# Kernel optimization log

Measured on AMD Instinct MI355X. Metric: run time of the kernel, lower is better.

The kernel has to match this reference:

```python
import jax, jax.numpy as jnp
import numpy as np

H = 128          # hid_feats
IN0, IN1 = 128, 64
OUT = 64         # out_feats
L = 3            # num_layers
N = 50000        # nodes per graph


def _rbf(x, W, b):
    # sklearn RBFSampler: z = sqrt(2/D) * cos(x @ W + b)
    return jnp.sqrt(2.0 / H) * jnp.cos(x @ W + b)


def _sage_branch(feat, src, dst, Wself, Wneigh, bias, n_nodes):
    # deg of each dst node (constant across layers)
    deg = jax.ops.segment_sum(jnp.ones_like(dst, dtype=feat.dtype), dst, n_nodes)
    denom = jnp.maximum(deg, 1.0)[:, None]
    for i in range(Wself.shape[0]):
        s = jax.ops.segment_sum(feat[src], dst, n_nodes)   # gather + scatter-add
        neigh = jnp.where(deg[:, None] > 0, s / denom, 0.0)
        feat = feat @ Wself[i] + neigh @ Wneigh[i] + bias[i]
    return feat


def setup_inputs() -> dict:
    key = jax.random.key(0)
    ks = jax.random.split(key, 20)
    gamma = 0.1
    inp = {}
    inp['feat0'] = jax.random.normal(ks[0], (N, IN0), jnp.float32)
    inp['feat1'] = jax.random.normal(ks[1], (N, IN1), jnp.float32)
    E = 800000
    inp['src0'] = jax.random.randint(ks[2], (E,), 0, N, jnp.int32)
    inp['dst0'] = jax.random.randint(ks[3], (E,), 0, N, jnp.int32)
    inp['src1'] = jax.random.randint(ks[4], (E,), 0, N, jnp.int32)
    inp['dst1'] = jax.random.randint(ks[5], (E,), 0, N, jnp.int32)
    # RBF random Fourier feature params (W ~ sqrt(2*gamma)*N(0,1), b ~ U[0,2pi))
    inp['rbf_W0'] = jnp.sqrt(2 * gamma) * jax.random.normal(ks[6], (IN0, H), jnp.float32)
    inp['rbf_b0'] = jax.random.uniform(ks[7], (H,), jnp.float32, 0.0, 2 * np.pi)
    inp['rbf_W1'] = jnp.sqrt(2 * gamma) * jax.random.normal(ks[8], (IN1, H), jnp.float32)
    inp['rbf_b1'] = jax.random.uniform(ks[9], (H,), jnp.float32, 0.0, 2 * np.pi)
    sc = 1.0 / np.sqrt(H)
    # branch 1 (g1) and branch 2 (g0) SAGEConv params, stacked over layers
    inp['Wself1'] = sc * jax.random.normal(ks[10], (L, H, H), jnp.float32)
    inp['Wneigh1'] = sc * jax.random.normal(ks[11], (L, H, H), jnp.float32)
    inp['b1'] = jnp.zeros((L, H), jnp.float32)
    inp['Wself2'] = sc * jax.random.normal(ks[12], (L, H, H), jnp.float32)
    inp['Wneigh2'] = sc * jax.random.normal(ks[13], (L, H, H), jnp.float32)
    inp['b2'] = jnp.zeros((L, H), jnp.float32)
    inp['fc1_W'] = sc * jax.random.normal(ks[14], (2 * H, H), jnp.float32)
    inp['fc1_b'] = jnp.zeros((H,), jnp.float32)
    inp['out_W'] = sc * jax.random.normal(ks[15], (H, OUT), jnp.float32)
    inp['out_b'] = jnp.zeros((OUT,), jnp.float32)
    inp['ro_W'] = (1.0 / np.sqrt(OUT)) * jax.random.normal(ks[16], (OUT, 1), jnp.float32)
    inp['ro_b'] = jnp.zeros((1,), jnp.float32)
    return inp


def reference(feat0, feat1, src0, dst0, src1, dst1,
              rbf_W0, rbf_b0, rbf_W1, rbf_b1,
              Wself1, Wneigh1, b1, Wself2, Wneigh2, b2,
              fc1_W, fc1_b, out_W, out_b, ro_W, ro_b):
    # branch 1: g1 path-complex features
    h1 = _rbf(feat1, rbf_W1, rbf_b1)
    y1 = _sage_branch(h1, src1, dst1, Wself1, Wneigh1, b1, feat1.shape[0])
    # branch 2: g0 node features
    h0 = _rbf(feat0, rbf_W0, rbf_b0)
    y2 = _sage_branch(h0, src0, dst0, Wself2, Wneigh2, b2, feat0.shape[0])
    # adaptive_avg_pool1d to 1 == mean over nodes
    y = jnp.concatenate([y2.mean(axis=0), y1.mean(axis=0)], axis=0)  # [2H]
    h = jax.nn.relu(y @ fc1_W + fc1_b)          # dropout is identity in eval
    h = jax.nn.leaky_relu(h @ out_W + out_b, negative_slope=0.01)
    return h @ ro_W + ro_b                      # [1]
```

## Files before the change

### kernel.cpp

```cpp
#include <hip/hip_runtime.h>
#include <math.h>

#define HF   128
#define CAPW 64
#define HB   64

__global__ __launch_bounds__(256) void hist_kernel(const int* __restrict__ s0, const int* __restrict__ d0,
                                                   const int* __restrict__ s1, const int* __restrict__ d1,
                                                   unsigned int* __restrict__ cntbuf,
                                                   int N, int E){
  __shared__ unsigned int sm32[12544];
  const int t = threadIdx.x;
  const int HW = (N + 3) >> 2;
  const int b  = blockIdx.x & 63;
  const int br = (blockIdx.x >> 6) & 1;
  const int z  = blockIdx.x >> 7;
  const int* keys = z ? (br ? d1 : d0) : (br ? s1 : s0);
  for (int w = t; w < HW; w += 256) sm32[w] = 0u;
  __syncthreads();
  const int C  = (E + HB - 1) / HB;
  const int lo = b * C;
  int hi = lo + C; if (hi > E) hi = E;
  for (int i = lo + t; i < hi; i += 256){
    int k = keys[i];
    atomicAdd(&sm32[k >> 2], 1u << ((k & 3) << 3));
  }
  __syncthreads();
  unsigned int* out = cntbuf + ((size_t)(z * 2 + br) * HB + b) * HW;
  for (int w = t; w < HW; w += 256) out[w] = sm32[w];
}

__global__ __launch_bounds__(256) void scan_kernel(unsigned int* __restrict__ cntbuf,
                                                   int* __restrict__ deg,
                                                   int* __restrict__ fill, int N){
  int k = blockIdx.x * 256 + threadIdx.x;
  if (k >= 2 * N) return;
  const int br = k >= N;
  const int kk = k - br * N;
  const int HW = (N + 3) >> 2;
  unsigned char* cb = (unsigned char*)cntbuf;
  size_t dbase = ((size_t)(2 + br) * HB) * HW * 4 + kk;
  int ds = 0;
  for (int b = 0; b < HB; ++b) ds += cb[dbase + (size_t)b * HW * 4];
  deg[k] = ds;
  size_t sbase = ((size_t)(0 + br) * HB) * HW * 4 + kk;
  int run = 0;
  for (int b = 0; b < HB; ++b){
    size_t a = sbase + (size_t)b * HW * 4;
    int c = cb[a];
    cb[a] = (unsigned char)run;
    run += c;
  }
  fill[k] = run;
}

__global__ __launch_bounds__(256) void scatter_kernel(const int* __restrict__ s0, const int* __restrict__ d0,
                                                      const int* __restrict__ s1, const int* __restrict__ d1,
                                                      const unsigned int* __restrict__ cntbuf,
                                                      unsigned short* __restrict__ slots,
                                                      int N, int E){
  __shared__ unsigned int sm32[12544];
  const int t  = threadIdx.x;
  const int b  = blockIdx.x & 63;
  const int br = blockIdx.x >> 6;
  const int HW = (N + 3) >> 2;
  const unsigned int* offw = cntbuf + ((size_t)br * HB + b) * HW;
  for (int w = t; w < HW; w += 256) sm32[w] = offw[w];
  __syncthreads();
  const int* srcA = br ? s1 : s0;
  const int* dstA = br ? d1 : d0;
  const int C  = (E + HB - 1) / HB;
  const int lo = b * C;
  int hi = lo + C; if (hi > E) hi = E;
  const size_t obase = (size_t)br * N;
  for (int i = lo + t; i < hi; i += 256){
    int s = srcA[i];
    int d = dstA[i];
    unsigned int old = atomicAdd(&sm32[s >> 2], 1u << ((s & 3) << 3));
    int j = (old >> ((s & 3) << 3)) & 0xff;
    if (j < CAPW) slots[(obase + s) * CAPW + j] = (unsigned short)d;
  }
}

__global__ __launch_bounds__(256) void pull1_kernel(const unsigned short* __restrict__ slots,
                                                    const int* __restrict__ fill,
                                                    const int* __restrict__ deg,
                                                    float* __restrict__ w1,
                                                    float* __restrict__ qa,
                                                    double* __restrict__ S, int N){
  int i = blockIdx.x * 256 + threadIdx.x;
  int t = threadIdx.x;
  float a = 0.f;
  int dgi = 0;
  int br = 0;
  bool valid = i < 2 * N;
  if (valid){
    br = i >= N;
    int o = br * N;
    int c = fill[i]; if (c > CAPW) c = CAPW;
    const unsigned short* sl = slots + (size_t)i * CAPW;
    int j = 0;
    for (; j + 7 < c; j += 8){
      int dA = sl[j], dB = sl[j+1], dC = sl[j+2], dD = sl[j+3];
      int dE = sl[j+4], dF = sl[j+5], dG = sl[j+6], dH = sl[j+7];
      a += 1.f/(float)deg[o+dA] + 1.f/(float)deg[o+dB]
         + 1.f/(float)deg[o+dC] + 1.f/(float)deg[o+dD]
         + 1.f/(float)deg[o+dE] + 1.f/(float)deg[o+dF]
         + 1.f/(float)deg[o+dG] + 1.f/(float)deg[o+dH];
    }
    for (; j < c; ++j) a += 1.f/(float)deg[o + sl[j]];
    dgi = deg[i];
    w1[i] = a;
    qa[i] = dgi > 0 ? a * (1.f/(float)dgi) : 0.f;
  }
  __shared__ double rd[4][256];
  bool pos = valid && dgi > 0;
  rd[0][t] = (pos && !br) ? 1.0 : 0.0;
  rd[1][t] = (pos && !br) ? (double)a : 0.0;
  rd[2][t] = (pos &&  br) ? 1.0 : 0.0;
  rd[3][t] = (pos &&  br) ? (double)a : 0.0;
  __syncthreads();
  for (int off = 128; off; off >>= 1){
    if (t < off){
      rd[0][t] += rd[0][t+off]; rd[1][t] += rd[1][t+off];
      rd[2][t] += rd[2][t+off]; rd[3][t] += rd[3][t+off];
    }
    __syncthreads();
  }
  if (t < 4) atomicAdd(&S[t], rd[t][0]);
}

template<bool WQ>
__global__ __launch_bounds__(256) void pull_kernel(const unsigned short* __restrict__ slots,
                                                   const int* __restrict__ fill,
                                                   const int* __restrict__ deg,
                                                   const float* __restrict__ qin,
                                                   float* __restrict__ wout,
                                                   float* __restrict__ qout, int N){
  int i = blockIdx.x * 256 + threadIdx.x;
  if (i >= 2 * N) return;
  int br = i >= N;
  int o = br * N;
  int c = fill[i]; if (c > CAPW) c = CAPW;
  const unsigned short* sl = slots + (size_t)i * CAPW;
  float a = 0.f;
  int j = 0;
  for (; j + 7 < c; j += 8){
    int dA = sl[j], dB = sl[j+1], dC = sl[j+2], dD = sl[j+3];
    int dE = sl[j+4], dF = sl[j+5], dG = sl[j+6], dH = sl[j+7];
    a += qin[o+dA] + qin[o+dB] + qin[o+dC] + qin[o+dD]
       + qin[o+dE] + qin[o+dF] + qin[o+dG] + qin[o+dH];
  }
  for (; j < c; ++j) a += qin[o + sl[j]];
  wout[i] = a;
  if (WQ){
    int dgi = deg[i];
    qout[i] = dgi > 0 ? a * (1.f/(float)dgi) : 0.f;
  }
}

template<int K1>
__device__ __forceinline__ void gemmred_body(const float* __restrict__ A,
                                             const float* __restrict__ W,
                                             const float* __restrict__ bias,
                                             const float* __restrict__ w1,
                                             const float* __restrict__ w2,
                                             const float* __restrict__ w3,
                                             int wo, float* __restrict__ partial,
                                             int rb, int N,
                                             float (*As)[68], float (*Bs)[132], float (*red)[128]){
  const int t  = threadIdx.x;
  const int tx = t & 15;
  const int ty = t >> 4;
  const int rowbase = rb << 6;

  float acc[4][8];
  #pragma unroll
  for (int i = 0; i < 4; ++i)
    #pragma unroll
    for (int j = 0; j < 8; ++j) acc[i][j] = 0.f;

  const int ar = t >> 2;
  const int ac = (t & 3) << 2;
  const int arow = rowbase + ar;
  const int bk0 = t >> 5;
  const int bc0 = (t & 31) << 2;

  for (int k0 = 0; k0 < K1; k0 += 16){
    __syncthreads();
    float4 av = make_float4(0.f, 0.f, 0.f, 0.f);
    if (arow < N) av = *(const float4*)&A[(size_t)arow * K1 + (k0 + ac)];
    As[ac + 0][ar] = av.x; As[ac + 1][ar] = av.y;
    As[ac + 2][ar] = av.z; As[ac + 3][ar] = av.w;
    float4 b0 = *(const float4*)&W[(size_t)(k0 + bk0) * HF + bc0];
    float4 b1 = *(const float4*)&W[(size_t)(k0 + bk0 + 8) * HF + bc0];
    *(float4*)&Bs[bk0][bc0]     = b0;
    *(float4*)&Bs[bk0 + 8][bc0] = b1;
    __syncthreads();
    #pragma unroll
    for (int kk = 0; kk < 16; ++kk){
      const float4 a  = *(const float4*)&As[kk][ty << 2];
      const float4 p0 = *(const float4*)&Bs[kk][tx << 2];
      const float4 p1 = *(const float4*)&Bs[kk][64 + (tx << 2)];
      const float aa[4] = {a.x, a.y, a.z, a.w};
      const float bb[8] = {p0.x, p0.y, p0.z, p0.w, p1.x, p1.y, p1.z, p1.w};
      #pragma unroll
      for (int i = 0; i < 4; ++i)
        #pragma unroll
        for (int j = 0; j < 8; ++j)
          acc[i][j] = fmaf(aa[i], bb[j], acc[i][j]);
    }
  }

  const float4 bia0 = *(const float4*)&bias[tx << 2];
  const float4 bia1 = *(const float4*)&bias[64 + (tx << 2)];
  const float bb0[8] = {bia0.x, bia0.y, bia0.z, bia0.w, bia1.x, bia1.y, bia1.z, bia1.w};
  float o[4][8];
  float wr[4][4];
  #pragma unroll
  for (int i = 0; i < 4; ++i){
    int row = rowbase + (ty << 2) + i;
    bool valid = row < N;
    #pragma unroll
    for (int j = 0; j < 8; ++j)
      o[i][j] = 0.125f * cosf(acc[i][j] + bb0[j]);
    wr[0][i] = valid ? 1.f : 0.f;
    wr[1][i] = valid ? w1[wo + row] : 0.f;
    wr[2][i] = valid ? w2[wo + row] : 0.f;
    wr[3][i] = valid ? w3[wo + row] : 0.f;
  }
  __syncthreads();
  #pragma unroll
  for (int k = 0; k < 4; ++k){
    float cw[8];
    #pragma unroll
    for (int j = 0; j < 8; ++j)
      cw[j] = wr[k][0]*o[0][j] + wr[k][1]*o[1][j] + wr[k][2]*o[2][j] + wr[k][3]*o[3][j];
    #pragma unroll
    for (int j = 0; j < 4; ++j){
      red[ty][(tx << 2) + j]      = cw[j];
      red[ty][64 + (tx << 2) + j] = cw[4 + j];
    }
    __syncthreads();
    for (int off = 8; off; off >>= 1){
      if (ty < off){
        #pragma unroll
        for (int j = 0; j < 4; ++j){
          red[ty][(tx << 2) + j]      += red[ty + off][(tx << 2) + j];
          red[ty][64 + (tx << 2) + j] += red[ty + off][64 + (tx << 2) + j];
        }
      }
      __syncthreads();
    }
    if (ty == 0){
      #pragma unroll
      for (int j = 0; j < 4; ++j){
        partial[(size_t)rb * 512 + k * 128 + (tx << 2) + j]      = red[0][(tx << 2) + j];
        partial[(size_t)rb * 512 + k * 128 + 64 + (tx << 2) + j] = red[0][64 + (tx << 2) + j];
      }
    }
    __syncthreads();
  }
}

__global__ __launch_bounds__(256) void gemmred2_kernel(const float* __restrict__ A0,
                                                       const float* __restrict__ W0,
                                                       const float* __restrict__ b0,
                                                       const float* __restrict__ A1,
                                                       const float* __restrict__ W1,
                                                       const float* __restrict__ b1,
                                                       const float* __restrict__ w1,
                                                       const float* __restrict__ w2,
                                                       const float* __restrict__ w3,
                                                       float* __restrict__ partial,
                                                       int N, int gg){
  __shared__ __align__(16) float smem[3200];
  float (*As)[68]   = (float(*)[68])smem;
  float (*Bs)[132]  = (float(*)[132])(smem + 1088);
  float (*red)[128] = (float(*)[128])smem;
  if ((int)blockIdx.x < gg)
    gemmred_body<128>(A0, W0, b0, w1, w2, w3, 0, partial, blockIdx.x, N, As, Bs, red);
  else
    gemmred_body<64>(A1, W1, b1, w1, w2, w3, N, partial + (size_t)gg * 512,
                     blockIdx.x - gg, N, As, Bs, red);
}

__global__ __launch_bounds__(512) void greduce_kernel(const float* __restrict__ partial,
                                                      double* __restrict__ G, int nb, int stride){
  int br = blockIdx.y;
  const float* p = partial + (size_t)br * stride;
  double* Gb = G + 512 * br;
  int t = threadIdx.x;
  double s = 0.0;
  for (int b = blockIdx.x; b < nb; b += gridDim.x) s += (double)p[(size_t)b * 512 + t];
  atomicAdd(&Gb[t], s);
}

__global__ __launch_bounds__(512) void head_kernel(const double* __restrict__ G,
                                                   const double* __restrict__ S,
                                                   const float* __restrict__ WsA, const float* __restrict__ WnA, const float* __restrict__ bA,
                                                   const float* __restrict__ WsB, const float* __restrict__ WnB, const float* __restrict__ bB,
                                                   float* __restrict__ ymean, int n){
  const int br = blockIdx.x;
  const double* Gb = G + 512 * br;
  const double* Sb = S + 2 * br;
  const float* Ws   = br ? WsB : WsA;
  const float* Wn   = br ? WnB : WnA;
  const float* bias = br ? bB  : bA;
  float* yout = ymean + 128 * br;

  __shared__ double g[4][128], ng[3][128];
  __shared__ float lws[32][128], lwn[32][128];
  const int t = threadIdx.x;
  const int k = t >> 7, j = t & 127;
  g[k][j] = Gb[t];
  double s[4];
  s[0] = (double)n; s[1] = Sb[0]; s[2] = Sb[1]; s[3] = 0.0;

  for (int i = 0; i < 3; ++i){
    const float* ws = Ws + (size_t)i * 16384;
    const float* wn = Wn + (size_t)i * 16384;
    const float* bi = bias + (size_t)i * 128;
    const int kmax = 2 - i;
    double a = (k <= kmax) ? s[k] * (double)bi[j] : 0.0;
    for (int mc = 0; mc < 128; mc += 32){
      __syncthreads();
      #pragma unroll
      for (int pp = 0; pp < 2; ++pp){
        int idx = (pp * 512 + t) << 2;
        int mm = idx >> 7, cc = idx & 127;
        *(float4*)&lws[mm][cc] = *(const float4*)&ws[(size_t)(mc + mm) * 128 + cc];
        *(float4*)&lwn[mm][cc] = *(const float4*)&wn[(size_t)(mc + mm) * 128 + cc];
      }
      __syncthreads();
      if (k <= kmax){
        #pragma unroll
        for (int m = 0; m < 32; ++m){
          a += g[k][mc + m]     * (double)lws[m][j];
          a += g[k + 1][mc + m] * (double)lwn[m][j];
        }
      }
    }
    __syncthreads();
    if (k <= kmax) ng[k][j] = a;
    __syncthreads();
    if (k <= kmax) g[k][j] = ng[k][j];
  }
  __syncthreads();
  if (t < 128) yout[t] = (float)(g[0][t] / (double)n);
}

__global__ void final_kernel(const float* __restrict__ ymean,
                             const float* __restrict__ fc1W, const float* __restrict__ fc1b,
                             const float* __restrict__ outW, const float* __restrict__ outb,
                             const float* __restrict__ roW, const float* __restrict__ rob,
                             float* __restrict__ out){
  __shared__ float y[256], h1[128], h2[64];
  int t = threadIdx.x;
  y[t] = ymean[t];
  __syncthreads();
  if (t < 128){
    float a = fc1b[t];
    for (int k = 0; k < 256; ++k) a = fmaf(y[k], fc1W[k * 128 + t], a);
    h1[t] = a > 0.f ? a : 0.f;
  }
  __syncthreads();
  if (t < 64){
    float a = outb[t];
    for (int k = 0; k < 128; ++k) a = fmaf(h1[k], outW[k * 64 + t], a);
    h2[t] = a > 0.f ? a : 0.01f * a;
  }
  __syncthreads();
  if (t == 0){
    float a = rob[0];
    for (int k = 0; k < 64; ++k) a = fmaf(h2[k], roW[k], a);
    out[0] = a;
  }
}

extern "C" void kernel_launch(void* const* d_in, const int* in_sizes, int n_in,
                              void* d_out, int out_size, void* d_ws, size_t ws_size,
                              hipStream_t stream){
  const float* feat0  = (const float*)d_in[0];
  const float* feat1  = (const float*)d_in[1];
  const int*   src0   = (const int*)d_in[2];
  const int*   dst0   = (const int*)d_in[3];
  const int*   src1   = (const int*)d_in[4];
  const int*   dst1   = (const int*)d_in[5];
  const float* rbfW0  = (const float*)d_in[6];
  const float* rbfb0  = (const float*)d_in[7];
  const float* rbfW1  = (const float*)d_in[8];
  const float* rbfb1  = (const float*)d_in[9];
  const float* Wself1 = (const float*)d_in[10];
  const float* Wneigh1= (const float*)d_in[11];
  const float* b1     = (const float*)d_in[12];
  const float* Wself2 = (const float*)d_in[13];
  const float* Wneigh2= (const float*)d_in[14];
  const float* b2     = (const float*)d_in[15];
  const float* fc1W   = (const float*)d_in[16];
  const float* fc1b   = (const float*)d_in[17];
  const float* outW   = (const float*)d_in[18];
  const float* outb   = (const float*)d_in[19];
  const float* roW    = (const float*)d_in[20];
  const float* rob    = (const float*)d_in[21];

  const int N = in_sizes[0] / 128;
  const int E = in_sizes[2];
  const int HW = (N + 3) >> 2;

  char* w = (char*)d_ws;
  size_t off = 0;
  auto alloc = [&](size_t bytes) -> char* {
    char* p = w + off; off += (bytes + 255) & ~(size_t)255; return p;
  };
  int*    deg    = (int*)   alloc((size_t)2 * N * 4);
  int*    fill   = (int*)   alloc((size_t)2 * N * 4);
  float*  w1     = (float*) alloc((size_t)2 * N * 4);
  float*  w2     = (float*) alloc((size_t)2 * N * 4);
  float*  w3     = (float*) alloc((size_t)2 * N * 4);
  float*  qa     = (float*) alloc((size_t)2 * N * 4);
  float*  qb     = (float*) alloc((size_t)2 * N * 4);
  double* S      = (double*)alloc(4 * sizeof(double));
  double* G      = (double*)alloc(1024 * sizeof(double));
  float*  ymean  = (float*) alloc(256 * sizeof(float));
  const int gg   = (N + 63) >> 6;
  float*  partial= (float*) alloc((size_t)2 * gg * 512 * 4);
  unsigned short* slots = (unsigned short*)alloc((size_t)2 * N * CAPW * 2);
  unsigned int* cntbuf  = (unsigned int*)alloc((size_t)4 * HB * HW * 4);

  const size_t slen = (size_t)((char*)ymean - (char*)S);

  const int nGrid2 = (2 * N + 255) >> 8;

  hipMemsetAsync(S, 0, slen, stream);
  hist_kernel<<<256, 256, 0, stream>>>(src0, dst0, src1, dst1, cntbuf, N, E);
  scan_kernel<<<nGrid2, 256, 0, stream>>>(cntbuf, deg, fill, N);
  scatter_kernel<<<128, 256, 0, stream>>>(src0, dst0, src1, dst1, cntbuf, slots, N, E);
  pull1_kernel<<<nGrid2, 256, 0, stream>>>(slots, fill, deg, w1, qa, S, N);
  pull_kernel<true ><<<nGrid2, 256, 0, stream>>>(slots, fill, deg, qa, w2, qb, N);
  pull_kernel<false><<<nGrid2, 256, 0, stream>>>(slots, fill, deg, qb, w3, qb, N);
  gemmred2_kernel<<<2 * gg, 256, 0, stream>>>(feat0, rbfW0, rbfb0, feat1, rbfW1, rbfb1,
                                              w1, w2, w3, partial, N, gg);
  greduce_kernel<<<dim3(16, 2), 512, 0, stream>>>(partial, G, gg, gg * 512);
  head_kernel<<<2, 512, 0, stream>>>(G, S, Wself2, Wneigh2, b2, Wself1, Wneigh1, b1, ymean, N);
  final_kernel<<<1, 256, 0, stream>>>(ymean, fc1W, fc1b, outW, outb, roW, rob, (float*)d_out);
}
```

Before: 216.2 us.

## Split scatter by source-key halves and enlarge RBF GEMM tile to 128 rows

The scatter kernel now launches twice as many blocks, and each block handles only half of the source-node key range. This halves the shared-memory offset table, which should allow more resident blocks, at the cost of every block reading all edges and skipping those outside its half. The fused RBF GEMM+reduction now processes 128-row tiles with an 8x8 per-thread accumulator, and the weighted reduction is accumulated directly in registers. This halves the number of partial blocks and gives more FMA work per shared-memory load, but raises register pressure.

```diff
diff --git a/kernel.cpp b/kernel.cpp
--- a/kernel.cpp
+++ b/kernel.cpp
@@ -59,13 +59,18 @@
                                                       const unsigned int* __restrict__ cntbuf,
                                                       unsigned short* __restrict__ slots,
                                                       int N, int E){
-  __shared__ unsigned int sm32[12544];
+  __shared__ unsigned int sm32[6272];
   const int t  = threadIdx.x;
   const int b  = blockIdx.x & 63;
-  const int br = blockIdx.x >> 6;
+  const int br = (blockIdx.x >> 6) & 1;
+  const int h  = blockIdx.x >> 7;
   const int HW = (N + 3) >> 2;
-  const unsigned int* offw = cntbuf + ((size_t)br * HB + b) * HW;
-  for (int w = t; w < HW; w += 256) sm32[w] = offw[w];
+  const int HN = ((N + 7) >> 3) << 2;
+  const int klo = h ? HN : 0;
+  const int khi = h ? N : HN;
+  const int nw  = (khi - klo + 3) >> 2;
+  const unsigned int* offw = cntbuf + ((size_t)br * HB + b) * HW + (klo >> 2);
+  for (int w = t; w < nw; w += 256) sm32[w] = offw[w];
   __syncthreads();
   const int* srcA = br ? s1 : s0;
   const int* dstA = br ? d1 : d0;
@@ -75,9 +80,11 @@
   const size_t obase = (size_t)br * N;
   for (int i = lo + t; i < hi; i += 256){
     int s = srcA[i];
+    if (s < klo || s >= khi) continue;
     int d = dstA[i];
-    unsigned int old = atomicAdd(&sm32[s >> 2], 1u << ((s & 3) << 3));
-    int j = (old >> ((s & 3) << 3)) & 0xff;
+    int sl = s - klo;
+    unsigned int old = atomicAdd(&sm32[sl >> 2], 1u << ((sl & 3) << 3));
+    int j = (old >> ((sl & 3) << 3)) & 0xff;
     if (j < CAPW) slots[(obase + s) * CAPW + j] = (unsigned short)d;
   }
 }
@@ -168,44 +175,50 @@
                                              const float* __restrict__ w3,
                                              int wo, float* __restrict__ partial,
                                              int rb, int N,
-                                             float (*As)[68], float (*Bs)[132], float (*red)[128]){
+                                             float (*As)[132], float (*Bs)[132], float (*red)[128]){
   const int t  = threadIdx.x;
   const int tx = t & 15;
   const int ty = t >> 4;
-  const int rowbase = rb << 6;
-
-  float acc[4][8];
+  const int rowbase = rb << 7;
+
+  float acc[8][8];
   #pragma unroll
-  for (int i = 0; i < 4; ++i)
+  for (int i = 0; i < 8; ++i)
     #pragma unroll
     for (int j = 0; j < 8; ++j) acc[i][j] = 0.f;
 
-  const int ar = t >> 2;
-  const int ac = (t & 3) << 2;
+  const int ar  = t >> 1;
+  const int ac8 = (t & 1) << 3;
   const int arow = rowbase + ar;
-  const int bk0 = t >> 5;
-  const int bc0 = (t & 31) << 2;
+  const int bk0 = t >> 4;
+  const int bc0 = (t & 15) << 3;
 
   for (int k0 = 0; k0 < K1; k0 += 16){
     __syncthreads();
-    float4 av = make_float4(0.f, 0.f, 0.f, 0.f);
-    if (arow < N) av = *(const float4*)&A[(size_t)arow * K1 + (k0 + ac)];
-    As[ac + 0][ar] = av.x; As[ac + 1][ar] = av.y;
-    As[ac + 2][ar] = av.z; As[ac + 3][ar] = av.w;
+    float4 av0 = make_float4(0.f,0.f,0.f,0.f), av1 = make_float4(0.f,0.f,0.f,0.f);
+    if (arow < N){
+      av0 = *(const float4*)&A[(size_t)arow * K1 + (k0 + ac8)];
+      av1 = *(const float4*)&A[(size_t)arow * K1 + (k0 + ac8 + 4)];
+    }
+    As[ac8 + 0][ar] = av0.x; As[ac8 + 1][ar] = av0.y;
+    As[ac8 + 2][ar] = av0.z; As[ac8 + 3][ar] = av0.w;
+    As[ac8 + 4][ar] = av1.x; As[ac8 + 5][ar] = av1.y;
+    As[ac8 + 6][ar] = av1.z; As[ac8 + 7][ar] = av1.w;
     float4 b0 = *(const float4*)&W[(size_t)(k0 + bk0) * HF + bc0];
-    float4 b1 = *(const float4*)&W[(size_t)(k0 + bk0 + 8) * HF + bc0];
+    float4 b1 = *(const float4*)&W[(size_t)(k0 + bk0) * HF + bc0 + 4];
     *(float4*)&Bs[bk0][bc0]     = b0;
-    *(float4*)&Bs[bk0 + 8][bc0] = b1;
+    *(float4*)&Bs[bk0][bc0 + 4] = b1;
     __syncthreads();
     #pragma unroll
     for (int kk = 0; kk < 16; ++kk){
-      const float4 a  = *(const float4*)&As[kk][ty << 2];
+      const float4 a0 = *(const float4*)&As[kk][ty << 2];
+      const float4 a1 = *(const float4*)&As[kk][64 + (ty << 2)];
       const float4 p0 = *(const float4*)&Bs[kk][tx << 2];
       const float4 p1 = *(const float4*)&Bs[kk][64 + (tx << 2)];
-      const float aa[4] = {a.x, a.y, a.z, a.w};
+      const float aa[8] = {a0.x, a0.y, a0.z, a0.w, a1.x, a1.y, a1.z, a1.w};
       const float bb[8] = {p0.x, p0.y, p0.z, p0.w, p1.x, p1.y, p1.z, p1.w};
       #pragma unroll
-      for (int i = 0; i < 4; ++i)
+      for (int i = 0; i < 8; ++i)
         #pragma unroll
         for (int j = 0; j < 8; ++j)
           acc[i][j] = fmaf(aa[i], bb[j], acc[i][j]);
@@ -215,31 +228,35 @@
   const float4 bia0 = *(const float4*)&bias[tx << 2];
   const float4 bia1 = *(const float4*)&bias[64 + (tx << 2)];
   const float bb0[8] = {bia0.x, bia0.y, bia0.z, bia0.w, bia1.x, bia1.y, bia1.z, bia1.w};
-  float o[4][8];
-  float wr[4][4];
+  float cw[4][8];
   #pragma unroll
-  for (int i = 0; i < 4; ++i){
-    int row = rowbase + (ty << 2) + i;
+  for (int k = 0; k < 4; ++k)
+    #pragma unroll
+    for (int j = 0; j < 8; ++j) cw[k][j] = 0.f;
+  #pragma unroll
+  for (int i = 0; i < 8; ++i){
+    int row = rowbase + (i < 4 ? (ty << 2) + i : 64 + (ty << 2) + (i - 4));
     bool valid = row < N;
+    float wk0 = valid ? 1.f : 0.f;
+    float wk1 = valid ? w1[wo + row] : 0.f;
+    float wk2 = valid ? w2[wo + row] : 0.f;
+    float wk3 = valid ? w3[wo + row] : 0.f;
     #pragma unroll
-    for (int j = 0; j < 8; ++j)
-      o[i][j] = 0.125f * cosf(acc[i][j] + bb0[j]);
-    wr[0][i] = valid ? 1.f : 0.f;
-    wr[1][i] = valid ? w1[wo + row] : 0.f;
-    wr[2][i] = valid ? w2[wo + row] : 0.f;
-    wr[3][i] = valid ? w3[wo + row] : 0.f;
+    for (int j = 0; j < 8; ++j){
+      float o = 0.125f * cosf(acc[i][j] + bb0[j]);
+      cw[0][j] = fmaf(wk0, o, cw[0][j]);
+      cw[1][j] = fmaf(wk1, o, cw[1][j]);
+      cw[2][j] = fmaf(wk2, o, cw[2][j]);
+      cw[3][j] = fmaf(wk3, o, cw[3][j]);
+    }
   }
   __syncthreads();
   #pragma unroll
   for (int k = 0; k < 4; ++k){
-    float cw[8];
-    #pragma unroll
-    for (int j = 0; j < 8; ++j)
-      cw[j] = wr[k][0]*o[0][j] + wr[k][1]*o[1][j] + wr[k][2]*o[2][j] + wr[k][3]*o[3][j];
     #pragma unroll
     for (int j = 0; j < 4; ++j){
-      red[ty][(tx << 2) + j]      = cw[j];
-      red[ty][64 + (tx << 2) + j] = cw[4 + j];
+      red[ty][(tx << 2) + j]      = cw[k][j];
+      red[ty][64 + (tx << 2) + j] = cw[k][4 + j];
     }
     __syncthreads();
     for (int off = 8; off; off >>= 1){
@@ -273,16 +290,16 @@
                                                        const float* __restrict__ w2,
                                                        const float* __restrict__ w3,
                                                        float* __restrict__ partial,
-                                                       int N, int gg){
-  __shared__ __align__(16) float smem[3200];
-  float (*As)[68]   = (float(*)[68])smem;
-  float (*Bs)[132]  = (float(*)[132])(smem + 1088);
+                                                       int N, int gBlk){
+  __shared__ __align__(16) float smem[4224];
+  float (*As)[132]  = (float(*)[132])smem;
+  float (*Bs)[132]  = (float(*)[132])(smem + 2112);
   float (*red)[128] = (float(*)[128])smem;
-  if ((int)blockIdx.x < gg)
+  if ((int)blockIdx.x < gBlk)
     gemmred_body<128>(A0, W0, b0, w1, w2, w3, 0, partial, blockIdx.x, N, As, Bs, red);
   else
-    gemmred_body<64>(A1, W1, b1, w1, w2, w3, N, partial + (size_t)gg * 512,
-                     blockIdx.x - gg, N, As, Bs, red);
+    gemmred_body<64>(A1, W1, b1, w1, w2, w3, N, partial + (size_t)gBlk * 512,
+                     blockIdx.x - gBlk, N, As, Bs, red);
 }
 
 __global__ __launch_bounds__(512) void greduce_kernel(const float* __restrict__ partial,
@@ -423,8 +440,8 @@
   double* S      = (double*)alloc(4 * sizeof(double));
   double* G      = (double*)alloc(1024 * sizeof(double));
   float*  ymean  = (float*) alloc(256 * sizeof(float));
-  const int gg   = (N + 63) >> 6;
-  float*  partial= (float*) alloc((size_t)2 * gg * 512 * 4);
+  const int gBlk = (N + 127) >> 7;
+  float*  partial= (float*) alloc((size_t)2 * gBlk * 512 * 4);
   unsigned short* slots = (unsigned short*)alloc((size_t)2 * N * CAPW * 2);
   unsigned int* cntbuf  = (unsigned int*)alloc((size_t)4 * HB * HW * 4);
 
@@ -435,13 +452,13 @@
   hipMemsetAsync(S, 0, slen, stream);
   hist_kernel<<<256, 256, 0, stream>>>(src0, dst0, src1, dst1, cntbuf, N, E);
   scan_kernel<<<nGrid2, 256, 0, stream>>>(cntbuf, deg, fill, N);
-  scatter_kernel<<<128, 256, 0, stream>>>(src0, dst0, src1, dst1, cntbuf, slots, N, E);
+  scatter_kernel<<<256, 256, 0, stream>>>(src0, dst0, src1, dst1, cntbuf, slots, N, E);
   pull1_kernel<<<nGrid2, 256, 0, stream>>>(slots, fill, deg, w1, qa, S, N);
   pull_kernel<true ><<<nGrid2, 256, 0, stream>>>(slots, fill, deg, qa, w2, qb, N);
   pull_kernel<false><<<nGrid2, 256, 0, stream>>>(slots, fill, deg, qb, w3, qb, N);
-  gemmred2_kernel<<<2 * gg, 256, 0, stream>>>(feat0, rbfW0, rbfb0, feat1, rbfW1, rbfb1,
-                                              w1, w2, w3, partial, N, gg);
-  greduce_kernel<<<dim3(16, 2), 512, 0, stream>>>(partial, G, gg, gg * 512);
+  gemmred2_kernel<<<2 * gBlk, 256, 0, stream>>>(feat0, rbfW0, rbfb0, feat1, rbfW1, rbfb1,
+                                                w1, w2, w3, partial, N, gBlk);
+  greduce_kernel<<<dim3(16, 2), 512, 0, stream>>>(partial, G, gBlk, gBlk * 512);
   head_kernel<<<2, 512, 0, stream>>>(G, S, Wself2, Wneigh2, b2, Wself1, Wneigh1, b1, ymean, N);
   final_kernel<<<1, 256, 0, stream>>>(ymean, fc1W, fc1b, outW, outb, roW, rob, (float*)d_out);
 }
```

Result: no change. 216.0 us (-0.1%).
